# Performance work log

Hardware: AMD Instinct MI355X
Metric: run time of the kernel (lower is better)

Reference implementation:

```python
import jax, jax.numpy as jnp
import numpy as np

B, N, E = 64, 20000, 160000
F_TEXT, HID, OUT = 300, 1024, 1664
NEG_SLOPE = 0.2


def setup_inputs() -> dict:
    key = jax.random.key(0)
    ks = jax.random.split(key, 9)
    img_feat = jax.random.normal(ks[0], (B, OUT), dtype=jnp.float32)
    node_features = jax.random.normal(ks[1], (N, F_TEXT), dtype=jnp.float32)
    edge_src = jax.random.randint(ks[2], (E,), 0, N, dtype=jnp.int32)
    edge_dst = jax.random.randint(ks[3], (E,), 0, N, dtype=jnp.int32)
    edge_weight = jax.random.uniform(ks[4], (E,), dtype=jnp.float32)
    W1 = jax.random.normal(ks[5], (F_TEXT, HID), dtype=jnp.float32) / np.sqrt(F_TEXT)
    b1 = jax.random.normal(ks[6], (HID,), dtype=jnp.float32) * 0.01
    W2 = jax.random.normal(ks[7], (HID, OUT), dtype=jnp.float32) / np.sqrt(HID)
    b2 = jax.random.normal(ks[8], (OUT,), dtype=jnp.float32) * 0.01
    return {"img_feat": img_feat, "node_features": node_features,
            "edge_src": edge_src, "edge_dst": edge_dst, "edge_weight": edge_weight,
            "W1": W1, "b1": b1, "W2": W2, "b2": b2}


def _gcn_norm(edge_src, edge_dst, edge_weight, num_nodes):
    # PyG gcn_norm with add_self_loops=False: symmetric degree normalization
    deg = jax.ops.segment_sum(edge_weight, edge_dst, num_segments=num_nodes)
    dinv = jnp.where(deg > 0, jax.lax.rsqrt(deg), 0.0)
    return dinv[edge_src] * edge_weight * dinv[edge_dst]


def _gcn_conv(x, edge_src, edge_dst, norm, W, b):
    # GCNConv: linear transform, then normalized gather -> scatter-add, then bias
    h = x @ W  # [N, out]
    msgs = h[edge_src] * norm[:, None]  # [E, out] gather + scale
    agg = jax.ops.segment_sum(msgs, edge_dst, num_segments=x.shape[0])
    return agg + b


def reference(img_feat, node_features, edge_src, edge_dst, edge_weight, W1, b1, W2, b2):
    num_nodes = node_features.shape[0]
    norm = _gcn_norm(edge_src, edge_dst, edge_weight, num_nodes)
    x = _gcn_conv(node_features, edge_src, edge_dst, norm, W1, b1)
    x = jnp.where(x >= 0, x, NEG_SLOPE * x)  # leaky_relu(0.2)
    x = _gcn_conv(x, edge_src, edge_dst, norm, W2, b2)
    return img_feat @ x.T  # [B, N]
```

## Files before the change

### kernel.cpp

```cpp
#include <hip/hip_runtime.h>
#include <hip/hip_bf16.h>

#define NNODES 20000
#define NEDGES 160000
#define BQ     64
#define FTEXT  300
#define KPAD1  320
#define HIDDIM 1024
#define OUTDIM 1664

typedef __attribute__((ext_vector_type(8))) short short8;
typedef __attribute__((ext_vector_type(4))) float floatx4;

__device__ inline unsigned short f2bf(float f) {
    union { float f; unsigned int u; } v; v.f = f;
    unsigned int r = v.u + 0x7FFF + ((v.u >> 16) & 1);
    return (unsigned short)(r >> 16);
}
__device__ inline float bf2f(unsigned short h) {
    union { unsigned int u; float f; } v; v.u = ((unsigned int)h) << 16;
    return v.f;
}

__device__ inline void gload16(const unsigned short* g, unsigned short* l) {
    __builtin_amdgcn_global_load_lds(
        (const __attribute__((address_space(1))) unsigned int*)g,
        (__attribute__((address_space(3))) unsigned int*)l, 16, 0, 0);
}

__global__ void degcnt_kernel(const int* __restrict__ dst, const float* __restrict__ w,
                              float* __restrict__ deg, int* __restrict__ cnt, int E) {
    int e = blockIdx.x * blockDim.x + threadIdx.x;
    if (e < E) {
        int d = dst[e];
        atomicAdd(&deg[d], w[e]);
        atomicAdd(&cnt[d], 1);
    }
}

__global__ __launch_bounds__(1024) void scan_kernel(const int* __restrict__ cnt,
                                                    int* __restrict__ row_start, int N) {
    __shared__ int partial[1024];
    const int CH = 20;
    int t = threadIdx.x;
    int begin = t * CH;
    int nloc = N - begin; if (nloc > CH) nloc = CH; if (nloc < 0) nloc = 0;
    int vals[CH];
    int s = 0;
    if (nloc == CH) {
        #pragma unroll
        for (int i = 0; i < CH / 4; i++) {
            int4 v = ((const int4*)(cnt + begin))[i];
            vals[i*4+0] = v.x; vals[i*4+1] = v.y; vals[i*4+2] = v.z; vals[i*4+3] = v.w;
            s += v.x + v.y + v.z + v.w;
        }
    } else {
        for (int i = 0; i < nloc; i++) { vals[i] = cnt[begin + i]; s += vals[i]; }
    }
    partial[t] = s;
    __syncthreads();
    for (int off = 1; off < 1024; off <<= 1) {
        int v = (t >= off) ? partial[t - off] : 0;
        __syncthreads();
        partial[t] += v;
        __syncthreads();
    }
    int run = (t == 0) ? 0 : partial[t - 1];
    for (int i = 0; i < nloc; i++) { row_start[begin + i] = run; run += vals[i]; }
    if (t == 1023) row_start[N] = partial[1023];
}

__global__ void fill_kernel(const int* __restrict__ dst, const int* __restrict__ src,
                            const float* __restrict__ w, const float* __restrict__ deg,
                            const int* __restrict__ row_start, int* __restrict__ cursor,
                            int* __restrict__ src_s, float* __restrict__ wnrm_s, int E) {
    int e = blockIdx.x * blockDim.x + threadIdx.x;
    if (e < E) {
        int d = dst[e], s = src[e];
        float dd = deg[d], ds = deg[s];
        float nv = (ds > 0.f ? rsqrtf(ds) : 0.f) * w[e] * (dd > 0.f ? rsqrtf(dd) : 0.f);
        int pos = row_start[d] + atomicAdd(&cursor[d], 1);
        src_s[pos] = s;
        wnrm_s[pos] = nv;
    }
}

__global__ __launch_bounds__(256) void aggnf_kernel(const unsigned short* __restrict__ nfb,
        const int* __restrict__ row_start, const int* __restrict__ src_s,
        const float* __restrict__ wnrm_s, unsigned short* __restrict__ out) {
    int wave = threadIdx.x >> 6, lane = threadIdx.x & 63;
    int d = blockIdx.x * 4 + wave;
    int s0 = row_start[d], s1 = row_start[d + 1];
    float4 acc  = make_float4(0.f, 0.f, 0.f, 0.f);
    float4 acc2 = make_float4(0.f, 0.f, 0.f, 0.f);
    for (int base = s0; base < s1; base += 64) {
        int m = s1 - base; if (m > 64) m = 64;
        int   src_l = (lane < m) ? src_s[base + lane]  : 0;
        float w_l   = (lane < m) ? wnrm_s[base + lane] : 0.f;
        int sj = __shfl(src_l, 0);
        float wj = __shfl(w_l, 0);
        const ushort4* row = (const ushort4*)(nfb + (long)sj * FTEXT);
        ushort4 hv  = row[lane];
        ushort4 hv2 = make_ushort4(0, 0, 0, 0);
        if (lane < 11) hv2 = row[64 + lane];
        for (int j = 0; j < m; j++) {
            ushort4 nv  = make_ushort4(0, 0, 0, 0);
            ushort4 nv2 = make_ushort4(0, 0, 0, 0);
            float wn = 0.f;
            if (j + 1 < m) {
                int sn = __shfl(src_l, j + 1);
                wn = __shfl(w_l, j + 1);
                const ushort4* nrow = (const ushort4*)(nfb + (long)sn * FTEXT);
                nv = nrow[lane];
                if (lane < 11) nv2 = nrow[64 + lane];
            }
            acc.x  += bf2f(hv.x)  * wj; acc.y  += bf2f(hv.y)  * wj;
            acc.z  += bf2f(hv.z)  * wj; acc.w  += bf2f(hv.w)  * wj;
            acc2.x += bf2f(hv2.x) * wj; acc2.y += bf2f(hv2.y) * wj;
            acc2.z += bf2f(hv2.z) * wj; acc2.w += bf2f(hv2.w) * wj;
            hv = nv; hv2 = nv2; wj = wn;
        }
    }
    unsigned short* orow = out + (long)d * KPAD1;
    ushort4 o;
    o.x = f2bf(acc.x); o.y = f2bf(acc.y); o.z = f2bf(acc.z); o.w = f2bf(acc.w);
    ((ushort4*)orow)[lane] = o;
    if (lane < 16) {
        ushort4 o2 = make_ushort4(0, 0, 0, 0);
        if (lane < 11) {
            o2.x = f2bf(acc2.x); o2.y = f2bf(acc2.y);
            o2.z = f2bf(acc2.z); o2.w = f2bf(acc2.w);
        }
        ((ushort4*)orow)[64 + lane] = o2;
    }
}

#define W1N  (HIDDIM * KPAD1)
#define N1F4 (HIDDIM * OUTDIM / 4)
#define N2F4 (BQ * OUTDIM / 4)
#define N3F4 (NNODES * FTEXT / 4)
__global__ void cvt_all_kernel(const float* __restrict__ W1, unsigned short* __restrict__ W1ch,
                               const float* __restrict__ W2, unsigned short* __restrict__ W2b,
                               const float* __restrict__ img, unsigned short* __restrict__ imgb,
                               const float* __restrict__ nf, unsigned short* __restrict__ nfb) {
    int i = blockIdx.x * 256 + threadIdx.x;
    if (i < W1N) {
        int c   = i >> 12;
        int w   = i & 4095;
        int lqg = w >> 10;
        int row = (w >> 3) & 127;
        int j   = i & 7;
        int nt = c / 10, s = c - nt * 10;
        int n = nt * 128 + row;
        int k = s * 32 + lqg * 8 + j;
        float v = (k < FTEXT) ? W1[(long)k * HIDDIM + n] : 0.f;
        W1ch[i] = f2bf(v);
        return;
    }
    i -= W1N;
    const float* in; unsigned short* outp; int j;
    if (i < N1F4)                    { in = W2;  outp = W2b;  j = i; }
    else if (i < N1F4 + N2F4)        { in = img; outp = imgb; j = i - N1F4; }
    else if (i < N1F4 + N2F4 + N3F4) { in = nf;  outp = nfb;  j = i - N1F4 - N2F4; }
    else return;
    float4 v = ((const float4*)in)[j];
    ushort4 o;
    o.x = f2bf(v.x); o.y = f2bf(v.y); o.z = f2bf(v.z); o.w = f2bf(v.w);
    ((ushort4*)outp)[j] = o;
}

__global__ __launch_bounds__(256) void ztcvec_kernel(const float* __restrict__ Ztf,
        unsigned short* __restrict__ Zt, const float* __restrict__ img,
        const float* __restrict__ b2, float* __restrict__ cvec) {
    if (blockIdx.x < (BQ * HIDDIM) / 256) {
        int i = blockIdx.x * 256 + threadIdx.x;
        Zt[i] = f2bf(Ztf[i]);
    } else {
        int b = blockIdx.x - (BQ * HIDDIM) / 256;
        int l = threadIdx.x;
        float v = 0.f;
        for (int f = l; f < OUTDIM; f += 256) v += img[(long)b * OUTDIM + f] * b2[f];
        __shared__ float red[256];
        red[l] = v;
        __syncthreads();
        if (l < 64) {
            v = red[l] + red[l + 64] + red[l + 128] + red[l + 192];
            for (int off = 32; off > 0; off >>= 1) v += __shfl_down(v, off);
            if (l == 0) cvec[b] = v;
        }
    }
}

template<int EPI, int OUT_BF16, int ATOMIC, int NT>
__global__ __launch_bounds__(256) void mfma_gemm(
        const unsigned short* __restrict__ A, const unsigned short* __restrict__ B,
        const float* __restrict__ bias, void* __restrict__ Cv,
        int M, int N, int K, int ldc) {
    constexpr int CT = NT / 16;
    __shared__ unsigned short As[128][40];
    __shared__ unsigned short Bs[NT][40];
    int t = threadIdx.x;
    int m0 = blockIdx.y * 128;
    int n0 = blockIdx.x * NT;
    int klen = K / gridDim.z;
    int kbeg = blockIdx.z * klen;
    int wave = t >> 6, lane = t & 63;
    int lm = lane & 15, lq = lane >> 4;
    floatx4 acc[2][CT] = {};
    for (int k0 = kbeg; k0 < kbeg + klen; k0 += 32) {
        #pragma unroll
        for (int p = 0; p < 2; p++) {
            int idx = p * 256 + t;
            int r = idx >> 2, c8 = (idx & 3) * 8;
            uint4 v = make_uint4(0, 0, 0, 0);
            int gm = m0 + r;
            if (gm < M) v = *(const uint4*)(A + (long)gm * K + k0 + c8);
            *(uint4*)&As[r][c8] = v;
        }
        #pragma unroll
        for (int p = 0; p < NT / 64; p++) {
            int idx = p * 256 + t;
            int r = idx >> 2, c8 = (idx & 3) * 8;
            uint4 v = *(const uint4*)(B + (long)(n0 + r) * K + k0 + c8);
            *(uint4*)&Bs[r][c8] = v;
        }
        __syncthreads();
        short8 a[2], b[CT];
        #pragma unroll
        for (int rt = 0; rt < 2; rt++)
            a[rt] = *(const short8*)&As[wave * 32 + rt * 16 + lm][lq * 8];
        #pragma unroll
        for (int ct = 0; ct < CT; ct++)
            b[ct] = *(const short8*)&Bs[ct * 16 + lm][lq * 8];
        #pragma unroll
        for (int rt = 0; rt < 2; rt++)
            #pragma unroll
            for (int ct = 0; ct < CT; ct++)
                acc[rt][ct] = __builtin_amdgcn_mfma_f32_16x16x32_bf16(
                    a[rt], b[ct], acc[rt][ct], 0, 0, 0);
        __syncthreads();
    }
    #pragma unroll
    for (int rt = 0; rt < 2; rt++) {
        #pragma unroll
        for (int r = 0; r < 4; r++) {
            int gm = m0 + wave * 32 + rt * 16 + lq * 4 + r;
            if (gm >= M) continue;
            #pragma unroll
            for (int ct = 0; ct < CT; ct++) {
                int gn = n0 + ct * 16 + lm;
                float v = acc[rt][ct][r];
                if (EPI) { v += bias[gn]; v = v >= 0.f ? v : 0.2f * v; }
                if (OUT_BF16)      ((unsigned short*)Cv)[(long)gm * ldc + gn] = f2bf(v);
                else if (ATOMIC)   atomicAdd((float*)Cv + (long)gm * ldc + gn, v);
                else               ((float*)Cv)[(long)gm * ldc + gn] = v;
            }
        }
    }
}

__global__ __launch_bounds__(256, 3) void xy_gemm(
        const unsigned short* __restrict__ aggNF, const unsigned short* __restrict__ W1ch,
        const float* __restrict__ b1, const unsigned short* __restrict__ Zt,
        float* __restrict__ Y, int M) {
    __shared__ unsigned short Bs[5][4096];
    __shared__ unsigned short xs[32][136];
    float (*ys)[68] = (float (*)[68])xs;
    int t = threadIdx.x;
    int wave = t >> 6, lane = t & 63;
    int lm = lane & 15, lq = lane >> 4;
    int wm = wave >> 1, wn = wave & 1;
    int m0 = blockIdx.x * 32;

    short8 afr[10];
    {
        const unsigned short* ap = aggNF + (long)(m0 + wm * 16 + lm) * KPAD1 + lq * 8;
        #pragma unroll
        for (int kk = 0; kk < 10; kk++)
            afr[kk] = *(const short8*)(ap + kk * 32);
    }
    #pragma unroll
    for (int c = 0; c < 3; c++) {
        const unsigned short* src = W1ch + (long)c * 4096 + t * 8;
        gload16(src,        &Bs[c][t * 8]);
        gload16(src + 2048, &Bs[c][2048 + t * 8]);
    }
    int cur = 0, nxt = 3;
    floatx4 yacc[4] = {};
    for (int nt = 0; nt < 8; nt++) {
        floatx4 acc[4] = {};
        for (int s = 0; s < 10; s++) {
            int c = nt * 10 + s;
            {
                const unsigned short* src = W1ch + (long)(c + 3) * 4096 + t * 8;
                gload16(src,        &Bs[nxt][t * 8]);
                gload16(src + 2048, &Bs[nxt][2048 + t * 8]);
            }
            asm volatile("s_waitcnt vmcnt(6)" ::: "memory");
            __builtin_amdgcn_s_barrier();
            __builtin_amdgcn_sched_barrier(0);
            short8 a = afr[s];
            #pragma unroll
            for (int ct = 0; ct < 4; ct++) {
                short8 b = *(const short8*)&Bs[cur][lq * 1024
                                                    + (wn * 64 + ct * 16 + lm) * 8];
                acc[ct] = __builtin_amdgcn_mfma_f32_16x16x32_bf16(a, b, acc[ct], 0, 0, 0);
            }
            cur = (cur + 1 == 5) ? 0 : cur + 1;
            nxt = (nxt + 1 == 5) ? 0 : nxt + 1;
        }
        #pragma unroll
        for (int ct = 0; ct < 4; ct++) {
            int col = wn * 64 + ct * 16 + lm;
            float bv = b1[nt * 128 + col];
            #pragma unroll
            for (int r = 0; r < 4; r++) {
                float v = acc[ct][r] + bv;
                v = v >= 0.f ? v : 0.2f * v;
                xs[wm * 16 + lq * 4 + r][col] = f2bf(v);
            }
        }
        #pragma unroll
        for (int kk2 = 0; kk2 < 2; kk2++) {
            short8 a = *(const short8*)&xs[wm * 16 + lm][wn * 64 + kk2 * 32 + lq * 8];
            #pragma unroll
            for (int bt = 0; bt < 4; bt++) {
                short8 b = *(const short8*)(Zt + (long)(bt * 16 + lm) * HIDDIM
                                                + nt * 128 + wn * 64 + kk2 * 32 + lq * 8);
                yacc[bt] = __builtin_amdgcn_mfma_f32_16x16x32_bf16(a, b, yacc[bt], 0, 0, 0);
            }
        }
    }
    __syncthreads();
    if (wn == 1) {
        #pragma unroll
        for (int bt = 0; bt < 4; bt++)
            #pragma unroll
            for (int r = 0; r < 4; r++)
                ys[wm * 16 + lq * 4 + r][bt * 16 + lm] = yacc[bt][r];
    }
    __syncthreads();
    if (wn == 0) {
        #pragma unroll
        for (int bt = 0; bt < 4; bt++)
            #pragma unroll
            for (int r = 0; r < 4; r++) {
                int row = wm * 16 + lq * 4 + r;
                Y[(long)(m0 + row) * 64 + bt * 16 + lm]
                    = yacc[bt][r] + ys[row][bt * 16 + lm];
            }
    }
}

__global__ __launch_bounds__(256) void outagg_kernel(const float* __restrict__ Y,
        const int* __restrict__ row_start, const int* __restrict__ src_s,
        const float* __restrict__ wnrm_s, const float* __restrict__ c,
        float* __restrict__ out, int N) {
    __shared__ float tile[4][68];
    int d0 = blockIdx.x * 4;
    int t = threadIdx.x;
    int wave = t >> 6, lane = t & 63;
    int d = d0 + wave;
    int s0 = row_start[d], s1 = row_start[d + 1];
    float acc = 0.f;
    for (int base = s0; base < s1; base += 64) {
        int m = s1 - base; if (m > 64) m = 64;
        int   src_l = (lane < m) ? src_s[base + lane]  : 0;
        float w_l   = (lane < m) ? wnrm_s[base + lane] : 0.f;
        int sj = __shfl(src_l, 0);
        float wj = __shfl(w_l, 0);
        float yv = Y[(long)sj * 64 + lane];
        for (int j = 0; j < m; j++) {
            float yn = 0.f, wn = 0.f;
            if (j + 1 < m) {
                int sn = __shfl(src_l, j + 1);
                wn = __shfl(w_l, j + 1);
                yn = Y[(long)sn * 64 + lane];
            }
            acc += wj * yv;
            yv = yn; wj = wn;
        }
    }
    tile[wave][lane] = acc + c[lane];
    __syncthreads();
    int b = t >> 2, j = t & 3;
    out[(long)b * N + d0 + j] = tile[j][b];
}

extern "C" void kernel_launch(void* const* d_in, const int* in_sizes, int n_in,
                              void* d_out, int out_size, void* d_ws, size_t ws_size,
                              hipStream_t stream) {
    const float* img_feat      = (const float*)d_in[0];
    const float* node_features = (const float*)d_in[1];
    const int*   edge_src      = (const int*)d_in[2];
    const int*   edge_dst      = (const int*)d_in[3];
    const float* edge_weight   = (const float*)d_in[4];
    const float* W1            = (const float*)d_in[5];
    const float* b1            = (const float*)d_in[6];
    const float* W2            = (const float*)d_in[7];
    const float* b2            = (const float*)d_in[8];
    float* out = (float*)d_out;

    const int N = NNODES, E = NEDGES;

    char* ws = (char*)d_ws;
    size_t off = 0;
    auto alloc = [&](size_t bytes) -> void* {
        void* p = ws + off;
        off = (off + bytes + 255) & ~(size_t)255;
        return p;
    };
    float*          deg       = (float*)alloc((size_t)N * 4);
    int*            cnt       = (int*)alloc((size_t)N * 4);
    int*            cursor    = (int*)alloc((size_t)N * 4);
    float*          Ztf       = (float*)alloc((size_t)BQ * HIDDIM * 4);
    size_t zero_bytes = off;
    float*          Y         = (float*)alloc((size_t)N * BQ * 4);
    int*            row_start = (int*)alloc((size_t)(N + 1) * 4);
    int*            src_s     = (int*)alloc((size_t)E * 4);
    float*          wnrm_s    = (float*)alloc((size_t)E * 4);
    unsigned short* aggNF     = (unsigned short*)alloc((size_t)N * KPAD1 * 2);
    unsigned short* W1ch      = (unsigned short*)alloc(((size_t)HIDDIM * KPAD1 + 3 * 4096) * 2);
    unsigned short* W2b       = (unsigned short*)alloc((size_t)HIDDIM * OUTDIM * 2);
    unsigned short* imgb      = (unsigned short*)alloc((size_t)BQ * OUTDIM * 2);
    unsigned short* nfb       = (unsigned short*)alloc((size_t)N * FTEXT * 2);
    unsigned short* Zt        = (unsigned short*)alloc((size_t)BQ * HIDDIM * 2);
    float*          cvec      = (float*)alloc((size_t)BQ * 4);

    hipMemsetAsync(ws, 0, zero_bytes, stream);

    int eb = (E + 255) / 256;
    degcnt_kernel<<<eb, 256, 0, stream>>>(edge_dst, edge_weight, deg, cnt, E);
    scan_kernel<<<1, 1024, 0, stream>>>(cnt, row_start, N);
    fill_kernel<<<eb, 256, 0, stream>>>(edge_dst, edge_src, edge_weight, deg, row_start,
                                        cursor, src_s, wnrm_s, E);

    cvt_all_kernel<<<(W1N + (N1F4 + N2F4 + N3F4) + 255) / 256, 256, 0, stream>>>(
        W1, W1ch, W2, W2b, img_feat, imgb, node_features, nfb);

    mfma_gemm<0, 0, 1, 64><<<dim3(HIDDIM / 64, 1, 13), 256, 0, stream>>>(
        imgb, W2b, nullptr, Ztf, BQ, HIDDIM, OUTDIM, HIDDIM);
    ztcvec_kernel<<<(BQ * HIDDIM) / 256 + BQ, 256, 0, stream>>>(Ztf, Zt, img_feat, b2, cvec);

    aggnf_kernel<<<N / 4, 256, 0, stream>>>(nfb, row_start, src_s, wnrm_s, aggNF);

    xy_gemm<<<dim3(NNODES / 32), 256, 0, stream>>>(aggNF, W1ch, b1, Zt, Y, N);

    outagg_kernel<<<N / 4, 256, 0, stream>>>(Y, row_start, src_s, wnrm_s, cvec, out, N);
}
```

Baseline: 230.2 us.

## Drop LDS staging of W1 in xy_gemm; load B fragments to registers with two-wave blocks

Rewrites xy_gemm to use 128-thread blocks where each wave covers both 16-row tiles. Each wave now loads its W1 fragments straight from global memory into registers, double-buffered in registers, in place of the async global-to-LDS ring buffer with a barrier on every k-step. This removes the per-step barriers and the LDS traffic, and each B fragment feeds two MFMAs. In exchange it uses more registers, has fewer waves per block, and W1 is fetched through L2 by every wave with no sharing across the block.

```diff
diff --git a/kernel.cpp b/kernel.cpp
--- a/kernel.cpp
+++ b/kernel.cpp
@@ -20,12 +20,6 @@
 __device__ inline float bf2f(unsigned short h) {
     union { unsigned int u; float f; } v; v.u = ((unsigned int)h) << 16;
     return v.f;
-}
-
-__device__ inline void gload16(const unsigned short* g, unsigned short* l) {
-    __builtin_amdgcn_global_load_lds(
-        (const __attribute__((address_space(1))) unsigned int*)g,
-        (__attribute__((address_space(3))) unsigned int*)l, 16, 0, 0);
 }
 
 __global__ void degcnt_kernel(const int* __restrict__ dst, const float* __restrict__ w,
@@ -259,96 +253,101 @@
     }
 }
 
-__global__ __launch_bounds__(256, 3) void xy_gemm(
+__global__ __launch_bounds__(128, 2) void xy_gemm(
         const unsigned short* __restrict__ aggNF, const unsigned short* __restrict__ W1ch,
         const float* __restrict__ b1, const unsigned short* __restrict__ Zt,
         float* __restrict__ Y, int M) {
-    __shared__ unsigned short Bs[5][4096];
     __shared__ unsigned short xs[32][136];
     float (*ys)[68] = (float (*)[68])xs;
     int t = threadIdx.x;
-    int wave = t >> 6, lane = t & 63;
+    int wn = t >> 6, lane = t & 63;
     int lm = lane & 15, lq = lane >> 4;
-    int wm = wave >> 1, wn = wave & 1;
     int m0 = blockIdx.x * 32;
 
-    short8 afr[10];
+    short8 afr[2][10];
+    #pragma unroll
+    for (int rt = 0; rt < 2; rt++) {
+        const unsigned short* ap = aggNF + (long)(m0 + rt * 16 + lm) * KPAD1 + lq * 8;
+        #pragma unroll
+        for (int kk = 0; kk < 10; kk++)
+            afr[rt][kk] = *(const short8*)(ap + kk * 32);
+    }
+    short8 bcur[4], bnxt[4];
     {
-        const unsigned short* ap = aggNF + (long)(m0 + wm * 16 + lm) * KPAD1 + lq * 8;
-        #pragma unroll
-        for (int kk = 0; kk < 10; kk++)
-            afr[kk] = *(const short8*)(ap + kk * 32);
-    }
-    #pragma unroll
-    for (int c = 0; c < 3; c++) {
-        const unsigned short* src = W1ch + (long)c * 4096 + t * 8;
-        gload16(src,        &Bs[c][t * 8]);
-        gload16(src + 2048, &Bs[c][2048 + t * 8]);
-    }
-    int cur = 0, nxt = 3;
-    floatx4 yacc[4] = {};
+        const unsigned short* bp = W1ch + lq * 1024 + (wn * 64 + lm) * 8;
+        #pragma unroll
+        for (int ct = 0; ct < 4; ct++) bcur[ct] = *(const short8*)(bp + ct * 128);
+    }
+    floatx4 yacc[2][4] = {};
     for (int nt = 0; nt < 8; nt++) {
-        floatx4 acc[4] = {};
+        floatx4 acc[2][4] = {};
+        #pragma unroll
         for (int s = 0; s < 10; s++) {
-            int c = nt * 10 + s;
-            {
-                const unsigned short* src = W1ch + (long)(c + 3) * 4096 + t * 8;
-                gload16(src,        &Bs[nxt][t * 8]);
-                gload16(src + 2048, &Bs[nxt][2048 + t * 8]);
-            }
-            asm volatile("s_waitcnt vmcnt(6)" ::: "memory");
-            __builtin_amdgcn_s_barrier();
-            __builtin_amdgcn_sched_barrier(0);
-            short8 a = afr[s];
-            #pragma unroll
-            for (int ct = 0; ct < 4; ct++) {
-                short8 b = *(const short8*)&Bs[cur][lq * 1024
-                                                    + (wn * 64 + ct * 16 + lm) * 8];
-                acc[ct] = __builtin_amdgcn_mfma_f32_16x16x32_bf16(a, b, acc[ct], 0, 0, 0);
-            }
-            cur = (cur + 1 == 5) ? 0 : cur + 1;
-            nxt = (nxt + 1 == 5) ? 0 : nxt + 1;
+            int c = nt * 10 + s + 1;
+            const unsigned short* bp = W1ch + (long)c * 4096 + lq * 1024
+                                            + (wn * 64 + lm) * 8;
+            #pragma unroll
+            for (int ct = 0; ct < 4; ct++) bnxt[ct] = *(const short8*)(bp + ct * 128);
+            #pragma unroll
+            for (int rt = 0; rt < 2; rt++)
+                #pragma unroll
+                for (int ct = 0; ct < 4; ct++)
+                    acc[rt][ct] = __builtin_amdgcn_mfma_f32_16x16x32_bf16(
+                        afr[rt][s], bcur[ct], acc[rt][ct], 0, 0, 0);
+            #pragma unroll
+            for (int ct = 0; ct < 4; ct++) bcur[ct] = bnxt[ct];
         }
         #pragma unroll
         for (int ct = 0; ct < 4; ct++) {
             int col = wn * 64 + ct * 16 + lm;
             float bv = b1[nt * 128 + col];
             #pragma unroll
-            for (int r = 0; r < 4; r++) {
-                float v = acc[ct][r] + bv;
-                v = v >= 0.f ? v : 0.2f * v;
-                xs[wm * 16 + lq * 4 + r][col] = f2bf(v);
+            for (int rt = 0; rt < 2; rt++)
+                #pragma unroll
+                for (int r = 0; r < 4; r++) {
+                    float v = acc[rt][ct][r] + bv;
+                    v = v >= 0.f ? v : 0.2f * v;
+                    xs[rt * 16 + lq * 4 + r][col] = f2bf(v);
+                }
+        }
+        __syncthreads();
+        #pragma unroll
+        for (int kk2 = 0; kk2 < 2; kk2++) {
+            #pragma unroll
+            for (int rt = 0; rt < 2; rt++) {
+                short8 a = *(const short8*)&xs[rt * 16 + lm][wn * 64 + kk2 * 32 + lq * 8];
+                #pragma unroll
+                for (int bt = 0; bt < 4; bt++) {
+                    short8 b = *(const short8*)(Zt + (long)(bt * 16 + lm) * HIDDIM
+                                                    + nt * 128 + wn * 64 + kk2 * 32 + lq * 8);
+                    yacc[rt][bt] = __builtin_amdgcn_mfma_f32_16x16x32_bf16(
+                        a, b, yacc[rt][bt], 0, 0, 0);
+                }
             }
         }
-        #pragma unroll
-        for (int kk2 = 0; kk2 < 2; kk2++) {
-            short8 a = *(const short8*)&xs[wm * 16 + lm][wn * 64 + kk2 * 32 + lq * 8];
-            #pragma unroll
-            for (int bt = 0; bt < 4; bt++) {
-                short8 b = *(const short8*)(Zt + (long)(bt * 16 + lm) * HIDDIM
-                                                + nt * 128 + wn * 64 + kk2 * 32 + lq * 8);
-                yacc[bt] = __builtin_amdgcn_mfma_f32_16x16x32_bf16(a, b, yacc[bt], 0, 0, 0);
-            }
-        }
-    }
-    __syncthreads();
+        __syncthreads();
+    }
     if (wn == 1) {
         #pragma unroll
-        for (int bt = 0; bt < 4; bt++)
-            #pragma unroll
-            for (int r = 0; r < 4; r++)
-                ys[wm * 16 + lq * 4 + r][bt * 16 + lm] = yacc[bt][r];
+        for (int rt = 0; rt < 2; rt++)
+            #pragma unroll
+            for (int bt = 0; bt < 4; bt++)
+                #pragma unroll
+                for (int r = 0; r < 4; r++)
+                    ys[rt * 16 + lq * 4 + r][bt * 16 + lm] = yacc[rt][bt][r];
     }
     __syncthreads();
     if (wn == 0) {
         #pragma unroll
-        for (int bt = 0; bt < 4; bt++)
-            #pragma unroll
-            for (int r = 0; r < 4; r++) {
-                int row = wm * 16 + lq * 4 + r;
-                Y[(long)(m0 + row) * 64 + bt * 16 + lm]
-                    = yacc[bt][r] + ys[row][bt * 16 + lm];
-            }
+        for (int rt = 0; rt < 2; rt++)
+            #pragma unroll
+            for (int bt = 0; bt < 4; bt++)
+                #pragma unroll
+                for (int r = 0; r < 4; r++) {
+                    int row = rt * 16 + lq * 4 + r;
+                    Y[(long)(m0 + row) * 64 + bt * 16 + lm]
+                        = yacc[rt][bt][r] + ys[row][bt * 16 + lm];
+                }
     }
 }
 
@@ -420,7 +419,7 @@
     int*            src_s     = (int*)alloc((size_t)E * 4);
     float*          wnrm_s    = (float*)alloc((size_t)E * 4);
     unsigned short* aggNF     = (unsigned short*)alloc((size_t)N * KPAD1 * 2);
-    unsigned short* W1ch      = (unsigned short*)alloc(((size_t)HIDDIM * KPAD1 + 3 * 4096) * 2);
+    unsigned short* W1ch      = (unsigned short*)alloc(((size_t)HIDDIM * KPAD1 + 4096) * 2);
     unsigned short* W2b       = (unsigned short*)alloc((size_t)HIDDIM * OUTDIM * 2);
     unsigned short* imgb      = (unsigned short*)alloc((size_t)BQ * OUTDIM * 2);
     unsigned short* nfb       = (unsigned short*)alloc((size_t)N * FTEXT * 2);
@@ -444,7 +443,7 @@
 
     aggnf_kernel<<<N / 4, 256, 0, stream>>>(nfb, row_start, src_s, wnrm_s, aggNF);
 
-    xy_gemm<<<dim3(NNODES / 32), 256, 0, stream>>>(aggNF, W1ch, b1, Zt, Y, N);
+    xy_gemm<<<dim3(NNODES / 32), 128, 0, stream>>>(aggNF, W1ch, b1, Zt, Y, N);
 
     outagg_kernel<<<N / 4, 256, 0, stream>>>(Y, row_start, src_s, wnrm_s, cvec, out, N);
 }
```

Result: slower. 245.8 us (+6.8%).

## Widen xy_gemm blocks to 80 rows and load whole W1 n-tiles per stage

Applied to the files above, without the earlier changes.

The fused X·W1 / Y GEMM now uses 640-thread blocks covering 80 node rows instead of 32, so each W1 tile fetched from global memory is shared by more rows. Instead of a 5-slot ring buffer refilled every k-step with a waitcnt and barrier, each full 128-column n-tile of W1 (80 KB of bf16) is loaded into LDS at once and refilled between n-tiles. This cuts per-k-step barriers and global traffic for W1, but uses much more LDS per block, which lowers occupancy. The next tile's load also overlaps only with the second-stage MFMA, so it is less pipelined. The epilogue that uses ys/xs must still match the 10-wave layout.

```diff
diff --git a/kernel.cpp b/kernel.cpp
--- a/kernel.cpp
+++ b/kernel.cpp
@@ -259,18 +259,18 @@
     }
 }
 
-__global__ __launch_bounds__(256, 3) void xy_gemm(
+__global__ __launch_bounds__(640) void xy_gemm(
         const unsigned short* __restrict__ aggNF, const unsigned short* __restrict__ W1ch,
         const float* __restrict__ b1, const unsigned short* __restrict__ Zt,
         float* __restrict__ Y, int M) {
-    __shared__ unsigned short Bs[5][4096];
-    __shared__ unsigned short xs[32][136];
+    __shared__ unsigned short Bsh[40960];
+    __shared__ unsigned short xs[80][136];
     float (*ys)[68] = (float (*)[68])xs;
     int t = threadIdx.x;
     int wave = t >> 6, lane = t & 63;
     int lm = lane & 15, lq = lane >> 4;
     int wm = wave >> 1, wn = wave & 1;
-    int m0 = blockIdx.x * 32;
+    int m0 = blockIdx.x * 80;
 
     short8 afr[10];
     {
@@ -279,35 +279,25 @@
         for (int kk = 0; kk < 10; kk++)
             afr[kk] = *(const short8*)(ap + kk * 32);
     }
-    #pragma unroll
-    for (int c = 0; c < 3; c++) {
-        const unsigned short* src = W1ch + (long)c * 4096 + t * 8;
-        gload16(src,        &Bs[c][t * 8]);
-        gload16(src + 2048, &Bs[c][2048 + t * 8]);
-    }
-    int cur = 0, nxt = 3;
+    {
+        const unsigned short* src = W1ch + t * 8;
+        #pragma unroll
+        for (int r = 0; r < 8; r++)
+            gload16(src + r * 5120, &Bsh[t * 8 + r * 5120]);
+    }
     floatx4 yacc[4] = {};
     for (int nt = 0; nt < 8; nt++) {
+        __syncthreads();
         floatx4 acc[4] = {};
+        #pragma unroll
         for (int s = 0; s < 10; s++) {
-            int c = nt * 10 + s;
-            {
-                const unsigned short* src = W1ch + (long)(c + 3) * 4096 + t * 8;
-                gload16(src,        &Bs[nxt][t * 8]);
-                gload16(src + 2048, &Bs[nxt][2048 + t * 8]);
-            }
-            asm volatile("s_waitcnt vmcnt(6)" ::: "memory");
-            __builtin_amdgcn_s_barrier();
-            __builtin_amdgcn_sched_barrier(0);
             short8 a = afr[s];
             #pragma unroll
             for (int ct = 0; ct < 4; ct++) {
-                short8 b = *(const short8*)&Bs[cur][lq * 1024
-                                                    + (wn * 64 + ct * 16 + lm) * 8];
+                short8 b = *(const short8*)&Bsh[s * 4096 + lq * 1024
+                                                + (wn * 64 + ct * 16 + lm) * 8];
                 acc[ct] = __builtin_amdgcn_mfma_f32_16x16x32_bf16(a, b, acc[ct], 0, 0, 0);
             }
-            cur = (cur + 1 == 5) ? 0 : cur + 1;
-            nxt = (nxt + 1 == 5) ? 0 : nxt + 1;
         }
         #pragma unroll
         for (int ct = 0; ct < 4; ct++) {
@@ -319,6 +309,13 @@
                 v = v >= 0.f ? v : 0.2f * v;
                 xs[wm * 16 + lq * 4 + r][col] = f2bf(v);
             }
+        }
+        __syncthreads();
+        if (nt + 1 < 8) {
+            const unsigned short* src = W1ch + (long)(nt + 1) * 40960 + t * 8;
+            #pragma unroll
+            for (int r = 0; r < 8; r++)
+                gload16(src + r * 5120, &Bsh[t * 8 + r * 5120]);
         }
         #pragma unroll
         for (int kk2 = 0; kk2 < 2; kk2++) {
@@ -420,7 +417,7 @@
     int*            src_s     = (int*)alloc((size_t)E * 4);
     float*          wnrm_s    = (float*)alloc((size_t)E * 4);
     unsigned short* aggNF     = (unsigned short*)alloc((size_t)N * KPAD1 * 2);
-    unsigned short* W1ch      = (unsigned short*)alloc(((size_t)HIDDIM * KPAD1 + 3 * 4096) * 2);
+    unsigned short* W1ch      = (unsigned short*)alloc((size_t)HIDDIM * KPAD1 * 2);
     unsigned short* W2b       = (unsigned short*)alloc((size_t)HIDDIM * OUTDIM * 2);
     unsigned short* imgb      = (unsigned short*)alloc((size_t)BQ * OUTDIM * 2);
     unsigned short* nfb       = (unsigned short*)alloc((size_t)N * FTEXT * 2);
@@ -444,7 +441,7 @@
 
     aggnf_kernel<<<N / 4, 256, 0, stream>>>(nfb, row_start, src_s, wnrm_s, aggNF);
 
-    xy_gemm<<<dim3(NNODES / 32), 256, 0, stream>>>(aggNF, W1ch, b1, Zt, Y, N);
+    xy_gemm<<<dim3(NNODES / 80), 640, 0, stream>>>(aggNF, W1ch, b1, Zt, Y, N);
 
     outagg_kernel<<<N / 4, 256, 0, stream>>>(Y, row_start, src_s, wnrm_s, cvec, out, N);
 }
```

After: 227.5 us. No clear change (-1.2%).
